# Optimization experiments

Measured on AMD Instinct MI355X. Metric: run time of the kernel, lower is better.

## Reference

```python
import jax, jax.numpy as jnp
import numpy as np

B, S, D, H = 2, 2048, 1024, 16
HD = D // H                      # head_dim = 64
F_POLY = HD + HD * HD            # 4160 degree-2 poly feature dim
M_HID = 2 * D                    # memory_expansion = 2
FFN_H = int(D * 4 * 2 / 3)       # 2730 SwiGLU hidden
GG_H = 64                        # gamma-gate hidden dim
EPS = 1e-6
OMEGA_W, OMEGA_DECAY = 64, 0.95
TTL_ALPHA, TTL_ETA, NS_ITERS = 0.999, 0.01, 5


def rmsnorm(x, w):
    return x * jax.lax.rsqrt(jnp.mean(x * x, -1, keepdims=True) + EPS) * w


def apply_rope(q, k):
    half = HD // 2
    inv = 1.0 / (10000.0 ** (jnp.arange(half, dtype=jnp.float32) / half))
    fr = jnp.arange(S, dtype=jnp.float32)[:, None] * inv[None, :]  # (S, half)
    cos, sin = jnp.cos(fr), jnp.sin(fr)
    def rot(x):
        x1, x2 = x[..., :half], x[..., half:]
        return jnp.concatenate([x1 * cos - x2 * sin, x1 * sin + x2 * cos], -1)
    return rot(q), rot(k)


def phi2(z):
    # degree-2 polynomial features: [z, vec(z z^T)/sqrt(d)]  -> capacity O(d_k^2)
    outer = (z[..., :, None] * z[..., None, :]).reshape(*z.shape[:-1], HD * HD)
    return jnp.concatenate([z, outer / jnp.sqrt(jnp.float32(HD))], -1)


def memory_forward(x, wk, w1, w2):
    feat = phi2(x @ wk)                     # (B,S,F_POLY)
    return jax.nn.silu(feat @ w1) @ w2      # (B,S,D)


def newton_schulz(G):
    # Muon-style quintic Newton-Schulz orthogonalization
    a, b, c = 3.4445, -4.7750, 2.0315
    X = G / (jnp.linalg.norm(G) + 1e-7)
    tall = X.shape[0] > X.shape[1]
    X = X.T if tall else X
    for _ in range(NS_ITERS):
        A = X @ X.T
        X = a * X + (b * A + c * (A @ A)) @ X
    return X.T if tall else X


def block_forward(x, norm1_w, norm2_w, qkv_w, q_norm_w, k_norm_w,
                  gamma_w1, gamma_w2, mem_wk, mem_w1, mem_w2,
                  memory_gate, wo_w, ffn_w1, ffn_w2, ffn_w3):
    h = rmsnorm(x, norm1_w)
    q, k, v = jnp.split(h @ qkv_w, 3, axis=-1)
    heads = lambda t: t.reshape(B, S, H, HD).transpose(0, 2, 1, 3)  # (B,H,S,HD)
    q, k, v = heads(q), heads(k), heads(v)
    q = rmsnorm(q, q_norm_w)   # qk-norm per head
    k = rmsnorm(k, k_norm_w)
    q, k = apply_rope(q, k)

    # input-dependent gamma gate (B,S,1)
    gamma = jax.nn.sigmoid(jax.nn.silu(h @ gamma_w1) @ gamma_w2)

    # causal QK memory projection: gamma-blended causal mean of keys
    k_cummean = jnp.cumsum(k, axis=2) / jnp.arange(1, S + 1, dtype=k.dtype)[None, None, :, None]
    g = gamma[:, None, :, :]                          # (B,1,S,1)
    q_mem = g * q + (1.0 - g) * k_cummean             # (B,H,S,HD)
    q_mem_flat = q_mem.transpose(0, 2, 1, 3).reshape(B, S, D)
    v_flat = v.transpose(0, 2, 1, 3).reshape(B, S, D)

    # --- TTL: Omega-rule loss + Newton-Schulz update of memory params ---
    pos = jnp.arange(S)
    dpow = jnp.float32(OMEGA_DECAY) ** (S - 1 - pos).astype(jnp.float32)
    dpow = jnp.where(pos >= S - OMEGA_W, dpow, 0.0)   # context-window pruning
    w_omega = gamma[..., 0] * dpow                    # (B,S)

    def omega_loss(wk, w1, w2):
        pred = memory_forward(q_mem_flat, wk, w1, w2)
        per_tok = jnp.sum((pred - v_flat) ** 2, -1)   # (B,S)
        return jnp.sum(w_omega * per_tok) / (jnp.sum(w_omega) + 1e-8)

    gk, g1, g2 = jax.grad(omega_loss, argnums=(0, 1, 2))(mem_wk, mem_w1, mem_w2)
    # momentum S_t = theta*0 + grad (fresh state), update M = alpha*M - eta*NS(S_t)
    mem_wk_u = TTL_ALPHA * mem_wk - TTL_ETA * newton_schulz(gk)
    mem_w1_u = TTL_ALPHA * mem_w1 - TTL_ETA * newton_schulz(g1)
    mem_w2_u = TTL_ALPHA * mem_w2 - TTL_ETA * newton_schulz(g2)

    # --- SWA branch (full causal attention) ---
    attn = jnp.einsum('bhsd,bhtd->bhst', q, k) * (HD ** -0.5)
    causal = jnp.tril(jnp.ones((S, S), dtype=bool))
    attn = jnp.where(causal, attn, -jnp.inf)
    attn = jax.nn.softmax(attn, -1)
    attn_out = jnp.einsum('bhst,bhtd->bhsd', attn, v)
    attn_out = attn_out.transpose(0, 2, 1, 3).reshape(B, S, D) @ wo_w

    # --- memory branch with learned output-level gate ---
    mem_out = memory_forward(q_mem_flat, mem_wk_u, mem_w1_u, mem_w2_u)
    mem_out = jax.nn.sigmoid(memory_gate) * mem_out

    x = x + attn_out + mem_out
    h2 = rmsnorm(x, norm2_w)
    x = x + (jax.nn.silu(h2 @ ffn_w1) * (h2 @ ffn_w3)) @ ffn_w2
    return x


def setup_inputs() -> dict:
    key = jax.random.key(0)
    ks = jax.random.split(key, 16)
    std = 0.02
    return {
        'x': jax.random.normal(ks[0], (B, S, D), jnp.float32),
        'norm1_w': jnp.ones((D,), jnp.float32),
        'norm2_w': jnp.ones((D,), jnp.float32),
        'qkv_w': jax.random.normal(ks[1], (D, 3 * D), jnp.float32) * std,
        'q_norm_w': jnp.ones((HD,), jnp.float32),
        'k_norm_w': jnp.ones((HD,), jnp.float32),
        'gamma_w1': jax.random.normal(ks[2], (D, GG_H), jnp.float32) * std,
        'gamma_w2': jnp.zeros((GG_H, 1), jnp.float32),  # zero-init -> gamma ~ 0.5
        'mem_wk': jax.random.normal(ks[3], (D, HD), jnp.float32) * std,
        'mem_w1': jax.random.normal(ks[4], (F_POLY, M_HID), jnp.float32) * std,
        'mem_w2': jax.random.normal(ks[5], (M_HID, D), jnp.float32) * std,
        'memory_gate': jnp.zeros((1,), jnp.float32),    # layer 0 -> pre-sigmoid 0.0
        'wo_w': jax.random.normal(ks[6], (D, D), jnp.float32) * (std / 2 ** 0.5),
        'ffn_w1': jax.random.normal(ks[7], (D, FFN_H), jnp.float32) * std,
        'ffn_w2': jax.random.normal(ks[8], (FFN_H, D), jnp.float32) * std,
        'ffn_w3': jax.random.normal(ks[9], (D, FFN_H), jnp.float32) * std,
    }


def reference(x, norm1_w, norm2_w, qkv_w, q_norm_w, k_norm_w, gamma_w1, gamma_w2,
              mem_wk, mem_w1, mem_w2, memory_gate, wo_w, ffn_w1, ffn_w2, ffn_w3):
    return block_forward(x, norm1_w, norm2_w, qkv_w, q_norm_w, k_norm_w,
                         gamma_w1, gamma_w2, mem_wk, mem_w1, mem_w2,
                         memory_gate, wo_w, ffn_w1, ffn_w2, ffn_w3)
```

## Files before the change

kernel.cpp:

```cpp
#include <hip/hip_runtime.h>
#include <math.h>

#define Bc 2
#define Sc 2048
#define Dc 1024
#define Hc 16
#define HDc 64
#define FPOLY 4160
#define MHID 2048
#define FFNH 2730
#define FFNHP 2752
#define GGH 64
#define NTOK 4096
#define NACT 128

typedef __bf16 bf16;
typedef __attribute__((ext_vector_type(8))) __bf16 bf16x8;
typedef __attribute__((ext_vector_type(4))) float f32x4;

#define AS1 __attribute__((address_space(1)))
#define AS3 __attribute__((address_space(3)))

__device__ __forceinline__ void gload16(const void* g, void* l) {
    __builtin_amdgcn_global_load_lds((AS1 const void*)g, (AS3 void*)l, 16, 0, 0);
// ... 66 lines not shown
    };
    stage(0, 0);
    __syncthreads();
    int buf = 0;
    for (int k0 = 32; k0 < K; k0 += 32) {
        stage(buf ^ 1, k0);
        compute(buf);
        __syncthreads();
        buf ^= 1;
    }
    compute(buf);
    const float amul = alpha * (sptr ? *sptr : 1.f);
#pragma unroll
    for (int nt = 0; nt < 4; ++nt) {
        const int col = bn + wn + nt * 16 + lrow;
        if (col >= N) continue;
#pragma unroll
        for (int mt = 0; mt < 4; ++mt) {
            const int rbase = bm + wm + mt * 16 + q * 4;
#pragma unroll
            for (int r = 0; r < 4; ++r) {
                const size_t o = (size_t)(rbase + r) * ldc + col;
                float v = amul * acc[mt][nt][r];
                if (beta != 0.f)
                    v += beta * (CINBF ? (float)((const bf16*)Cin)[o] : ((const float*)Cin)[o]);
                if (act == 1) v = v / (1.f + __expf(-v));
                if (OUTBF) ((bf16*)Cout)[o] = (bf16)v;
                else       ((float*)Cout)[o] = v;
            }
        }
    }
}

template<int OUTBF, int CINBF>
__global__ __launch_bounds__(256) void gemm_direct(
    const bf16* __restrict__ A, const bf16* __restrict__ Bt,
    const void* __restrict__ Cin, void* __restrict__ Cout,
    int M, int N, int K, int ldc,
    float alpha, float beta, int act, const float* __restrict__ sptr)
{
    const int tid = threadIdx.x, w = tid >> 6, lane = tid & 63;
    const int lrow = lane & 15, quad = lane >> 4;
    const int bm = blockIdx.y * 128 + w * 32;
    const int bn = blockIdx.x * 128;
    f32x4 acc[2][8];
#pragma unroll
    for (int mt = 0; mt < 2; ++mt)
#pragma unroll
        for (int nt = 0; nt < 8; ++nt) { acc[mt][nt][0] = 0.f; acc[mt][nt][1] = 0.f; acc[mt][nt][2] = 0.f; acc[mt][nt][3] = 0.f; }
    const bf16* Abase = A + (size_t)(bm + lrow) * K + quad * 8;
    const bf16* Bbase = Bt + (size_t)(bn + lrow) * K + quad * 8;
#pragma unroll 2
    for (int k0 = 0; k0 < K; k0 += 32) {
        bf16x8 af0 = *(const bf16x8*)(Abase + k0);
        bf16x8 af1 = *(const bf16x8*)(Abase + (size_t)16 * K + k0);
#pragma unroll
        for (int nt = 0; nt < 8; ++nt) {
            bf16x8 bfr = *(const bf16x8*)(Bbase + (size_t)nt * 16 * K + k0);
            acc[0][nt] = __builtin_amdgcn_mfma_f32_16x16x32_bf16(af0, bfr, acc[0][nt], 0, 0, 0);
            acc[1][nt] = __builtin_amdgcn_mfma_f32_16x16x32_bf16(af1, bfr, acc[1][nt], 0, 0, 0);
        }
    }
    const float amul = alpha * (sptr ? *sptr : 1.f);
#pragma unroll
    for (int nt = 0; nt < 8; ++nt) {
        const int col = bn + nt * 16 + lrow;
        if (col >= N) continue;
#pragma unroll
        for (int mt = 0; mt < 2; ++mt) {
            const int rbase = bm + mt * 16 + quad * 4;
#pragma unroll
            for (int r = 0; r < 4; ++r) {
                const int row = rbase + r;
                if (row >= M) continue;
                const size_t o = (size_t)row * ldc + col;
                float v = amul * acc[mt][nt][r];
                if (beta != 0.f)
                    v += beta * (CINBF ? (float)((const bf16*)Cin)[o] : ((const float*)Cin)[o]);
                if (act == 1) v = v / (1.f + __expf(-v));
                if (OUTBF) ((bf16*)Cout)[o] = (bf16)v;
                else       ((float*)Cout)[o] = v;
            }
        }
    }
}

__global__ __launch_bounds__(256) void gemm_skp(
    const bf16* __restrict__ A, const bf16* __restrict__ Bt,
    float* __restrict__ part, int M, int N, int K, int KC)
{
    const int tid = threadIdx.x, w = tid >> 6, lane = tid & 63;
    const int lrow = lane & 15, quad = lane >> 4;
    const int bm = blockIdx.y * 128 + w * 32;
    const int bn = blockIdx.x * 128;
    const int z = blockIdx.z;
    const int kb = z * KC;
    int ke = kb + KC; if (ke > K) ke = K;
    f32x4 acc[2][8];
#pragma unroll
    for (int mt = 0; mt < 2; ++mt)
#pragma unroll
        for (int nt = 0; nt < 8; ++nt) { acc[mt][nt][0] = 0.f; acc[mt][nt][1] = 0.f; acc[mt][nt][2] = 0.f; acc[mt][nt][3] = 0.f; }
    const bf16* Abase = A + (size_t)(bm + lrow) * K + quad * 8;
    const bf16* Bbase = Bt + (size_t)(bn + lrow) * K + quad * 8;
#pragma unroll 2
    for (int k0 = kb; k0 < ke; k0 += 32) {
        bf16x8 af0 = *(const bf16x8*)(Abase + k0);
        bf16x8 af1 = *(const bf16x8*)(Abase + (size_t)16 * K + k0);
#pragma unroll
        for (int nt = 0; nt < 8; ++nt) {
            bf16x8 bfr = *(const bf16x8*)(Bbase + (size_t)nt * 16 * K + k0);
            acc[0][nt] = __builtin_amdgcn_mfma_f32_16x16x32_bf16(af0, bfr, acc[0][nt], 0, 0, 0);
            acc[1][nt] = __builtin_amdgcn_mfma_f32_16x16x32_bf16(af1, bfr, acc[1][nt], 0, 0, 0);
        }
    }
    float* po = part + (size_t)z * M * N;
#pragma unroll
    for (int nt = 0; nt < 8; ++nt) {
        const int col = bn + nt * 16 + lrow;
        if (col >= N) continue;
#pragma unroll
        for (int mt = 0; mt < 2; ++mt) {
            const int rbase = bm + mt * 16 + quad * 4;
#pragma unroll
            for (int r = 0; r < 4; ++r) {
                const int row = rbase + r;
                if (row >= M) continue;
                po[(size_t)row * N + col] = acc[mt][nt][r];
            }
        }
    }
}

__global__ void skred(const float* __restrict__ part, float* __restrict__ out,
                      int SK, int MN)
{
    int i = blockIdx.x * 256 + threadIdx.x;
    if (i >= MN) return;
    float s = 0.f;
    for (int z = 0; z < SK; ++z) s += part[(size_t)z * MN + i];
    out[i] = s;
}

__global__ __launch_bounds__(256) void gram_bat(
    const bf16* __restrict__ X0, const bf16* __restrict__ X1,
    const bf16* __restrict__ X2, const bf16* __restrict__ X3,
    const bf16* __restrict__ X4, float* __restrict__ part)
{
    const int z = blockIdx.x, m = blockIdx.y;
    const bf16* A; int K;
    if      (m == 0) { A = X0; K = 2048; }
    else if (m == 1) { A = X1; K = 1024; }
    else if (m == 2) { A = X2; K = 2048; }
    else if (m == 3) { A = X3; K = 1024; }
    else             { A = X4; K = 64;   }
    if (z * 64 >= K) return;
    const int tid = threadIdx.x, w = tid >> 6, lane = tid & 63;
    const int lrow = lane & 15, quad = lane >> 4;
    const int bm = w * 32;
    f32x4 acc[2][8];
#pragma unroll
    for (int mt = 0; mt < 2; ++mt)
#pragma unroll
        for (int nt = 0; nt < 8; ++nt) { acc[mt][nt][0] = 0.f; acc[mt][nt][1] = 0.f; acc[mt][nt][2] = 0.f; acc[mt][nt][3] = 0.f; }
    const bf16* Abase = A + (size_t)(bm + lrow) * K + quad * 8;
    const bf16* Bbase = A + (size_t)lrow * K + quad * 8;
#pragma unroll 2
    for (int k0 = z * 64; k0 < z * 64 + 64; k0 += 32) {
        bf16x8 af0 = *(const bf16x8*)(Abase + k0);
        bf16x8 af1 = *(const bf16x8*)(Abase + (size_t)16 * K + k0);
#pragma unroll
        for (int nt = 0; nt < 8; ++nt) {
            bf16x8 bfr = *(const bf16x8*)(Bbase + (size_t)nt * 16 * K + k0);
            acc[0][nt] = __builtin_amdgcn_mfma_f32_16x16x32_bf16(af0, bfr, acc[0][nt], 0, 0, 0);
// ... 177 lines not shown
                for (int nt = 0; nt < 8; ++nt)
#pragma unroll
                    for (int r = 0; r < 4; ++r) {
                        const int row = bm + mt * 16 + quad * 4 + r, col = nt * 16 + lrow;
                        Fc[(size_t)row * 128 + col] = (bf16)acc[mt][nt][r];
                    }
        }
        gemm_ll(Cl, FTl);
#pragma unroll
        for (int mt = 0; mt < 2; ++mt)
#pragma unroll
            for (int nt = 0; nt < 8; ++nt)
#pragma unroll
                for (int r = 0; r < 4; ++r) {
                    const int row = bm + mt * 16 + quad * 4 + r, col = nt * 16 + lrow;
                    Ml[swz(col, row)] = (bf16)acc[mt][nt][r];
                }
        __syncthreads();
        gemm_ll(Ml, FTl);
#pragma unroll
        for (int mt = 0; mt < 2; ++mt)
#pragma unroll
            for (int nt = 0; nt < 8; ++nt)
#pragma unroll
                for (int r = 0; r < 4; ++r) {
                    const int row = bm + mt * 16 + quad * 4 + r, col = nt * 16 + lrow;
                    Cl[swz(row, col)] = (bf16)acc[mt][nt][r];
                }
        __syncthreads();
    }
}

__global__ __launch_bounds__(256) void tconv_kernel(
    const float* __restrict__ W, bf16* __restrict__ Wt, int K, int N, int Kpad)
{
    __shared__ float t[32][33];
    const int k0 = blockIdx.x * 32, n0 = blockIdx.y * 32;
    const int tx = threadIdx.x & 31, ty = threadIdx.x >> 5;
#pragma unroll
    for (int r = 0; r < 4; ++r) {
        int gk = k0 + ty + r * 8, gn = n0 + tx;
        t[ty + r * 8][tx] = (gk < K && gn < N) ? W[(size_t)gk * N + gn] : 0.f;
    }
    __syncthreads();
#pragma unroll
    for (int r = 0; r < 4; ++r) {
        int gn = n0 + ty + r * 8, gk = k0 + tx;
        if (gn < N && gk < Kpad) Wt[(size_t)gn * Kpad + gk] = (bf16)t[tx][ty + r * 8];
    }
}

__global__ __launch_bounds__(256) void tconv6_kernel(
    const float* __restrict__ s0, const float* __restrict__ s1,
    const float* __restrict__ s2, const float* __restrict__ s3,
    const float* __restrict__ s4, const float* __restrict__ s5,
    bf16* __restrict__ d0, bf16* __restrict__ d1, bf16* __restrict__ d2,
    bf16* __restrict__ d3, bf16* __restrict__ d4, bf16* __restrict__ d5)
{
    const int zz = blockIdx.z;
    const float* W; bf16* Wt; int N;
    if      (zz == 0) { W = s0; Wt = d0; N = 2048; }
    else if (zz == 1) { W = s1; Wt = d1; N = 1024; }
    else if (zz == 2) { W = s2; Wt = d2; N = 64;   }
    else if (zz == 3) { W = s3; Wt = d3; N = 1024; }
    else if (zz == 4) { W = s4; Wt = d4; N = 4160; }
    else              { W = s5; Wt = d5; N = 2048; }
    const int k0 = blockIdx.x * 32, n0 = blockIdx.y * 32;
    if (n0 >= N) return;
    __shared__ float t[32][33];
    const int tx = threadIdx.x & 31, ty = threadIdx.x >> 5;
#pragma unroll
    for (int r = 0; r < 4; ++r) {
        int gk = k0 + ty + r * 8, gn = n0 + tx;
        t[ty + r * 8][tx] = (gk < 128 && gn < N) ? W[(size_t)gk * N + gn] : 0.f;
    }
    __syncthreads();
#pragma unroll
    for (int r = 0; r < 4; ++r) {
        int gn = n0 + ty + r * 8, gk = k0 + tx;
        if (gn < N) Wt[(size_t)gn * 128 + gk] = (bf16)t[tx][ty + r * 8];
    }
}

__global__ void cvt_kernel(const float* __restrict__ in, bf16* __restrict__ out, int n)
{
    for (int i = blockIdx.x * 256 + threadIdx.x; i < n; i += gridDim.x * 256)
        out[i] = (bf16)in[i];
}

__global__ __launch_bounds__(256) void vtrans_kernel(
    const bf16* __restrict__ qkv, bf16* __restrict__ vt)
{
    __shared__ bf16 t[32][33];
    const int s0 = blockIdx.x * 32, d0 = blockIdx.y * 32, bh = blockIdx.z;
    const int b = bh >> 4, h = bh & 15;
    const int tx = threadIdx.x & 31, ty = threadIdx.x >> 5;
#pragma unroll
    for (int r = 0; r < 4; ++r) {
        int s = s0 + ty + r * 8;
        t[ty + r * 8][tx] = qkv[((size_t)b * Sc + s) * 3072 + 2048 + h * 64 + d0 + tx];
    }
    __syncthreads();
#pragma unroll
    for (int r = 0; r < 4; ++r) {
        int d = d0 + ty + r * 8;
        vt[((size_t)bh * 64 + d) * Sc + s0 + tx] = t[tx][ty + r * 8];
    }
}

__global__ __launch_bounds__(256) void rms_rows(
    const float* __restrict__ in, const float* __restrict__ w,
    bf16* __restrict__ out, int D)
{
    const int row = blockIdx.x;
    const float* r = in + (size_t)row * D;
    bf16* o = out + (size_t)row * D;
    float s = 0.f;
    for (int i = threadIdx.x; i < D; i += 256) { float v = r[i]; s += v * v; }
    __shared__ float red[256];
    red[threadIdx.x] = s;
    __syncthreads();
    for (int st = 128; st; st >>= 1) {
// ... 28 lines not shown
    const int h = y & 15, which = y >> 4;
    const float* w = which ? kw : qw;
    bf16* dst = which ? kd : qd;
    const size_t row = ((size_t)b * Sc + s) * 3072 + which * 1024 + h * 64;
    float v = (float)src[row + lane];
    float ss = v * v;
#pragma unroll
    for (int off = 32; off; off >>= 1) ss += __shfl_xor(ss, off);
    v = v * rsqrtf(ss / 64.f + 1e-6f) * w[lane];
    const int j = lane & 31;
    float inv = powf(10000.f, -(float)j / 32.f);
    float ang = (float)s * inv;
    float sn = sinf(ang), cs = cosf(ang);
    float p = __shfl_xor(v, 32);
    float o;
    if (lane < 32) o = v * cs - p * sn;
    else           o = p * sn + v * cs;
    const size_t od = (((size_t)b * Hc + h) * Sc + s) * 64 + lane;
    dst[od] = (bf16)o;
}

__global__ void kpsum_kernel(const bf16* __restrict__ kn, float* __restrict__ psum)
{
    const int bh = blockIdx.x, c = blockIdx.y, d = threadIdx.x;
    const size_t base = (size_t)bh * Sc * 64 + (size_t)c * 128 * 64 + d;
    float s = 0.f;
    for (int i = 0; i < 128; ++i) s += (float)kn[base + (size_t)i * 64];
    psum[((size_t)bh * 16 + c) * 64 + d] = s;
}

__global__ void qmem2_kernel(
    const bf16* __restrict__ qn, const bf16* __restrict__ kn,
    const float* __restrict__ gamma, const float* __restrict__ psum,
    float* __restrict__ qmem)
{
    const int bh = blockIdx.x, c = blockIdx.y;
    const int b = bh >> 4, hh = bh & 15;
    const int d = threadIdx.x;
    const size_t base = (size_t)bh * Sc * 64;
    float run = 0.f;
    for (int cc = 0; cc < c; ++cc) run += psum[((size_t)bh * 16 + cc) * 64 + d];
    for (int s = c * 128; s < c * 128 + 128; ++s) {
        run += (float)kn[base + (size_t)s * 64 + d];
        float cm = run / (float)(s + 1);
        float g = gamma[b * Sc + s];
        float qv = (float)qn[base + (size_t)s * 64 + d];
        qmem[((size_t)(b * Sc + s)) * Dc + hh * 64 + d] = g * qv + (1.f - g) * cm;
    }
}

__global__ __launch_bounds__(256, 4) void attn_mfma(
    const bf16* __restrict__ qn, const bf16* __restrict__ kn,
    const bf16* __restrict__ vt, bf16* __restrict__ outp)
{
    const int flat = blockIdx.x;
    const int glow = flat & 7, t2 = flat >> 3;
    const int xq = t2 & 31, ghigh = t2 >> 5;
    const int g = glow | (ghigh << 3);
    const int h = g & 15, b = g >> 4;
    const int bh = b * Hc + h;
    const int tid = threadIdx.x, w = tid >> 6, lane = tid & 63;
    const int lrow = lane & 15, quad = lane >> 4;
    const int rhalf = w & 1, pgrp = w >> 1;
    __shared__ bf16 Ps[4][16][136];
    __shared__ float Ob[2][16][68];
    __shared__ float Lb[2][16];
    const bf16* kbase = kn + (size_t)bh * Sc * 64;
    const bf16* vtb = vt + (size_t)bh * 64 * Sc;
    const float SC = 0.1803368801f;
#pragma unroll 1
    for (int ti = 0; ti < 2; ++ti) {
        const int zt = ti ? (63 - xq) : xq;
        const int qb = zt * 32;
        const int nc = (qb >> 7) + 1;
        const int par = pgrp ^ ti;
        const int rowg = qb + rhalf * 16 + quad * 4;
        bf16x8 qf[2];
        const bf16* qbase = qn + ((size_t)bh * Sc + qb + rhalf * 16) * 64;
#pragma unroll
        for (int ks = 0; ks < 2; ++ks)
// ... 110 lines not shown
    __shared__ float red[128];
    red[t] = v; __syncthreads();
    for (int st = 64; st; st >>= 1) { if (t < st) red[t] += red[t + st]; __syncthreads(); }
    if (t == 0) wsum[0] = red[0];
}

__global__ __launch_bounds__(256) void phi2_f32(
    const float* __restrict__ z, float* __restrict__ feat, bf16* __restrict__ featb)
{
    const int f = blockIdx.x * 256 + threadIdx.x;
    const int t = blockIdx.y;
    if (f >= FPOLY) return;
    const float* zr = z + (size_t)t * 64;
    float v;
    if (f < 64) v = zr[f];
    else { int i = (f - 64) >> 6, j = (f - 64) & 63; v = zr[i] * zr[j] * 0.125f; }
    feat[(size_t)t * FPOLY + f] = v;
    featb[(size_t)t * FPOLY + f] = (bf16)v;
}

__global__ __launch_bounds__(256) void phi2_bf16(
    const float* __restrict__ z, bf16* __restrict__ feat)
{
    const int f = blockIdx.x * 256 + threadIdx.x;
    const int t = blockIdx.y;
    if (f >= FPOLY) return;
    const float* zr = z + (size_t)t * 64;
    float v;
    if (f < 64) v = zr[f];
    else { int i = (f - 64) >> 6, j = (f - 64) & 63; v = zr[i] * zr[j] * 0.125f; }
    feat[(size_t)t * FPOLY + f] = (bf16)v;
}

__global__ void silu_kernel(const float* __restrict__ in, float* __restrict__ out,
                            bf16* __restrict__ outb, int n)
{
    int i = blockIdx.x * 256 + threadIdx.x;
    if (i < n) {
        float v = in[i];
        float s = v / (1.f + expf(-v));
        out[i] = s; outb[i] = (bf16)s;
    }
}

__global__ void dpred_kernel(const float* __restrict__ pred, const float* __restrict__ va,
                             const float* __restrict__ wvec, const float* __restrict__ wsum,
                             float* __restrict__ dpred, bf16* __restrict__ dpredb)
{
    int i = blockIdx.x * 256 + threadIdx.x;
    if (i < NACT * Dc) {
        int t = i >> 10;
        float v = 2.f * wvec[t] / (wsum[0] + 1e-8f) * (pred[i] - va[i]);
        dpred[i] = v; dpredb[i] = (bf16)v;
    }
}

__global__ void dsilu_kernel(const float* __restrict__ dsu, const float* __restrict__ u,
                             float* __restrict__ du, bf16* __restrict__ dub, int n)
{
    int i = blockIdx.x * 256 + threadIdx.x;
    if (i < n) {
        float uv = u[i];
        float sg = 1.f / (1.f + expf(-uv));
        float v = dsu[i] * sg * (1.f + uv * (1.f - sg));
        du[i] = v; dub[i] = (bf16)v;
    }
}

__global__ void dz_kernel(const float* __restrict__ dfeat, const float* __restrict__ za,
                          float* __restrict__ dz, bf16* __restrict__ dzb)
{
    const int t = blockIdx.x;
    const int k = threadIdx.x;
    const float* df = dfeat + (size_t)t * FPOLY;
    const float* z = za + (size_t)t * 64;
    float s1 = 0.f, s2 = 0.f;
    for (int j = 0; j < 64; ++j) {
        float zj = z[j];
        s1 += df[64 + k * 64 + j] * zj;
        s2 += df[64 + j * 64 + k] * zj;
    }
    float v = df[k] + 0.125f * (s1 + s2);
    dz[(size_t)t * 64 + k] = v;
    dzb[(size_t)t * 64 + k] = (bf16)v;
}

__global__ void sgate_kernel(const float* __restrict__ mg, float* __restrict__ out)
{
    out[0] = 1.f / (1.f + expf(-mg[0]));
}

__global__ void swiglu_pack(const bf16* __restrict__ u, bf16* __restrict__ o)
{
    int i = blockIdx.x * 256 + threadIdx.x;
    if (i >= NTOK * FFNHP) return;
    int t = i / FFNHP, k = i % FFNHP;
    if (k >= FFNH) { o[i] = (bf16)0.f; return; }
    float a = (float)u[(size_t)t * 5504 + k];
    float b = (float)u[(size_t)t * 5504 + 2752 + k];
    o[i] = (bf16)(a / (1.f + __expf(-a)) * b);
}
// ... 39 lines not shown
    float* x2 = (float*)slabBC;
    bf16* qmemb = (bf16*)slabD;
    bf16* t1b4  = (bf16*)slabD;
    bf16* attnb = (bf16*)slabF;
    bf16* hb = (bf16*)slabG;      bf16* mw1b = (bf16*)slabG;
    bf16* w1uT = (bf16*)slabG;    bf16* h2b = (bf16*)slabG;
    bf16* qkvb = (bf16*)takeB(25165824);
    bf16* ffpk = qkvb;

    bf16* qkvwT = (bf16*)takeB(6291456);
    bf16* gw1T  = (bf16*)takeB(262144);
    bf16* wowT  = (bf16*)takeB(2097152);
    bf16* mw1T  = (bf16*)takeB(17039360);
    bf16* mw2T  = (bf16*)takeB(4194304);
    bf16* fw13T = (bf16*)takeB(11272192);
    bf16* fw2T  = (bf16*)takeB(5636096);
    bf16* mw2b  = (bf16*)takeB(4194304);
    bf16* mwkTb = (bf16*)takeB(262144);
    bf16* wkuTb = (bf16*)takeB(262144);
    bf16* w2uT  = (bf16*)takeB(4194304);

    float* zf    = (float*)takeB(1048576);
    float* gg1   = (float*)takeB(1048576);
    float* gamma = (float*)takeB(16384);
    float* wvec  = (float*)takeB(512);
    float* scal  = (float*)takeB(256);
    float* psum  = (float*)takeB(131072);
    float* xa    = (float*)takeB(524288);
    float* va    = (float*)takeB(524288);
    float* za    = (float*)takeB(32768);
    float* featA = (float*)takeB(2129920);
    float* ua    = (float*)takeB(1048576);
    float* sua   = (float*)takeB(1048576);
    float* preda = (float*)takeB(524288);
    float* dpreda= (float*)takeB(524288);
    float* dsua  = (float*)takeB(1048576);
    float* dua   = (float*)takeB(1048576);
    float* dfeata= (float*)takeB(2129920);
    float* dza   = (float*)takeB(32768);
    float* SA    = (float*)takeB(196608);
    float* CA    = (float*)takeB(196608);
    bf16* featAb = (bf16*)takeB(1064960);
    bf16* suab   = (bf16*)takeB(524288);
    bf16* xab    = (bf16*)takeB(262144);
    bf16* duab   = (bf16*)takeB(524288);
    bf16* dpredab= (bf16*)takeB(262144);
    bf16* dzab   = (bf16*)takeB(16384);
    bf16* PT1Tb  = (bf16*)takeB(524288);
    bf16* PT2Tb  = (bf16*)takeB(262144);
    bf16* PT3Tb  = (bf16*)takeB(32768);
    bf16* duaTb  = (bf16*)takeB(524288);
    bf16* dpredaTb=(bf16*)takeB(262144);
    bf16* dzaTb  = (bf16*)takeB(32768);
    bf16* xaTb   = (bf16*)takeB(262144);
    bf16* featATb= (bf16*)takeB(1081344);
    bf16* suaTb  = (bf16*)takeB(524288);
    bf16* Sb16  = (bf16*)takeB(98304);
    bf16* Cb16  = (bf16*)takeB(98304);
    bf16* FcAb  = (bf16*)takeB(98304);
    bf16* FcTAb = (bf16*)takeB(98304);

    auto gemmB = [&](int outbf, int cinbf, const bf16* A, const bf16* Bt,
                     const void* Cin, void* C, int M, int N, int K, int ldc,
                     float alpha, float beta, int act, const float* sptr) {
        dim3 grid((N + 127) / 128, M / 128);
        if (outbf && cinbf) gemm_bt<1, 1><<<grid, 256, 0, stream>>>(A, Bt, Cin, C, M, N, K, ldc, alpha, beta, act, sptr);
        else if (outbf)     gemm_bt<1, 0><<<grid, 256, 0, stream>>>(A, Bt, Cin, C, M, N, K, ldc, alpha, beta, act, sptr);
        else                gemm_bt<0, 0><<<grid, 256, 0, stream>>>(A, Bt, Cin, C, M, N, K, ldc, alpha, beta, act, sptr);
    };
    auto gdir = [&](int outbf, int cinbf, const bf16* A, const bf16* Bt,
                    const void* Cin, void* C, int M, int N, int K, int ldc,
                    float alpha, float beta, int act, const float* sptr) {
        dim3 grid((N + 127) / 128, (M + 127) / 128);
        if (outbf && cinbf)      gemm_direct<1, 1><<<grid, 256, 0, stream>>>(A, Bt, Cin, C, M, N, K, ldc, alpha, beta, act, sptr);
        else if (outbf)          gemm_direct<1, 0><<<grid, 256, 0, stream>>>(A, Bt, Cin, C, M, N, K, ldc, alpha, beta, act, sptr);
        else if (cinbf)          gemm_direct<0, 1><<<grid, 256, 0, stream>>>(A, Bt, Cin, C, M, N, K, ldc, alpha, beta, act, sptr);
        else                     gemm_direct<0, 0><<<grid, 256, 0, stream>>>(A, Bt, Cin, C, M, N, K, ldc, alpha, beta, act, sptr);
    };
    auto skp = [&](const bf16* A, const bf16* Bt, float* out,
                   int M, int N, int K, int KC) {
        int SK = (K + KC - 1) / KC;
        gemm_skp<<<dim3((N + 127) / 128, (M + 127) / 128, SK), 256, 0, stream>>>(A, Bt, partA, M, N, K, KC);
        int MN = M * N;
        skred<<<(MN + 255) / 256, 256, 0, stream>>>(partA, out, SK, MN);
    };
    auto tconv = [&](const float* W, bf16* Wt, int K, int N, int Kpad) {
        tconv_kernel<<<dim3((Kpad + 31) / 32, (N + 31) / 32), 256, 0, stream>>>(W, Wt, K, N, Kpad);
    };

    tconv(qkvw, qkvwT, Dc, 3 * Dc, Dc);
    tconv(gw1, gw1T, Dc, GGH, Dc);
    tconv(wow, wowT, Dc, Dc, Dc);
    tconv(mw1, mw1T, FPOLY, MHID, FPOLY);
    tconv(mw2, mw2T, MHID, Dc, MHID);
    tconv(fw1, fw13T, Dc, FFNH, Dc);
    tconv(fw3, fw13T + (size_t)2752 * Dc, Dc, FFNH, Dc);
    tconv(fw2, fw2T, FFNH, Dc, FFNHP);
    tconv(mwk, mwkTb, Dc, HDc, Dc);
    cvt_kernel<<<2048, 256, 0, stream>>>(mw2, mw2b, MHID * Dc);
    sgate_kernel<<<1, 1, 0, stream>>>(mgate, scal + 2);

    rms_rows<<<NTOK, 256, 0, stream>>>(x, n1w, hb, Dc);
    gemmB(1, 0, hb, qkvwT, nullptr, qkvb, NTOK, 3 * Dc, Dc, 3 * Dc, 1.f, 0.f, 0, nullptr);
    snr_qk<<<dim3(Sc / 4, 32, Bc), 256, 0, stream>>>(qkvb, qnw, knw, qnb, knb);
    skp(hb, gw1T, gg1, NTOK, GGH, Dc, 256);
    gamma_kernel<<<NTOK / 4, 256, 0, stream>>>(gg1, gw2, gamma);
    cvt_kernel<<<2048, 256, 0, stream>>>(mw1, mw1b, FPOLY * MHID);

    vtrans_kernel<<<dim3(Sc / 32, 2, Bc * Hc), 256, 0, stream>>>(qkvb, vt);
    kpsum_kernel<<<dim3(Bc * Hc, 16), 64, 0, stream>>>(knb, psum);
    qmem2_kernel<<<dim3(Bc * Hc, 16), 64, 0, stream>>>(qnb, knb, gamma, psum, qmem);
    attn_mfma<<<dim3(1024), 256, 0, stream>>>(qnb, knb, vt, attnb);

    gather_active<<<NACT, 256, 0, stream>>>(qmem, qkvb, xa, xab, va);
    wvec_kernel<<<1, 128, 0, stream>>>(gamma, wvec, scal);

    skp(xab, mwkTb, za, NACT, HDc, Dc, 64);
    phi2_f32<<<dim3((FPOLY + 255) / 256, NACT), 256, 0, stream>>>(za, featA, featAb);
    skp(featAb, mw1T, ua, NACT, MHID, FPOLY, 288);
    silu_kernel<<<(NACT * MHID + 255) / 256, 256, 0, stream>>>(ua, sua, suab, NACT * MHID);
    skp(suab, mw2T, preda, NACT, Dc, MHID, 128);
    dpred_kernel<<<(NACT * Dc + 255) / 256, 256, 0, stream>>>(preda, va, wvec, scal, dpreda, dpredab);
    skp(dpredab, mw2b, dsua, NACT, MHID, Dc, 128);
    dsilu_kernel<<<(NACT * MHID + 255) / 256, 256, 0, stream>>>(dsua, ua, dua, duab, NACT * MHID);
    skp(duab, mw1b, dfeata, NACT, FPOLY, MHID, 256);
    dz_kernel<<<NACT, 64, 0, stream>>>(dfeata, za, dza, dzab);

    tconv6_kernel<<<dim3(4, 130, 6), 256, 0, stream>>>(
        dua, dpreda, dza, xa, featA, sua,
        duaTb, dpredaTb, dzaTb, xaTb, featATb, suaTb);

    gram_trick<<<1, 256, 0, stream>>>(za, SA);
    gram_bat<<<dim3(32, 5), 256, 0, stream>>>(suab, xab, duab, dpredab, dzab, partA);
    gram_red<<<320, 256, 0, stream>>>(partA, SA, CA);
    ns_norm_kernel<<<3, 256, 0, stream>>>(SA, CA, Sb16, Cb16, scal + 8);
    ns_fused<<<3, 256, 0, stream>>>(Sb16, Cb16, FcAb, FcTAb);
    gdir(1, 0, duaTb,    FcTAb,         nullptr, PT1Tb, MHID, 128, 128, 128, 1.f, 0.f, 0, scal + 8);
    gdir(1, 0, dpredaTb, FcTAb + 16384, nullptr, PT2Tb, Dc,   128, 128, 128, 1.f, 0.f, 0, scal + 9);
    gdir(1, 0, dzaTb,    FcTAb + 32768, nullptr, PT3Tb, HDc,  128, 128, 128, 1.f, 0.f, 0, scal + 10);

    gdir(1, 1, PT3Tb, xaTb, mwkTb, wkuTb, HDc, Dc, 128, Dc, -0.01f, 0.999f, 0, nullptr);
    gemmB(1, 1, PT1Tb, featATb, mw1T, w1uT, MHID, FPOLY, 128, FPOLY, -0.01f, 0.999f, 0, nullptr);
    gemmB(1, 1, PT2Tb, suaTb, mw2T, w2uT, Dc, MHID, 128, MHID, -0.01f, 0.999f, 0, nullptr);

    gemmB(0, 0, attnb, wowT, x, x2, NTOK, Dc, Dc, Dc, 1.f, 1.f, 0, nullptr);
    cvt_kernel<<<2048, 256, 0, stream>>>(qmem, qmemb, NTOK * Dc);
    gdir(0, 0, qmemb, wkuTb, nullptr, zf, NTOK, HDc, Dc, HDc, 1.f, 0.f, 0, nullptr);

    phi2_bf16<<<dim3((FPOLY + 255) / 256, NTOK), 256, 0, stream>>>(zf, featC4);
    gemmB(1, 0, featC4, w1uT, nullptr, t1b4, NTOK, MHID, FPOLY, MHID, 1.f, 0.f, 1, nullptr);
    gemmB(0, 0, t1b4, w2uT, x2, x2, NTOK, Dc, MHID, Dc, 1.f, 1.f, 0, scal + 2);

    rms_rows<<<NTOK, 256, 0, stream>>>(x2, n2w, h2b, Dc);
    gemmB(1, 0, h2b, fw13T, nullptr, ff13b, NTOK, 5482, Dc, 5504, 1.f, 0.f, 0, nullptr);
    swiglu_pack<<<(NTOK * FFNHP + 255) / 256, 256, 0, stream>>>(ff13b, ffpk);
    gemmB(0, 0, ffpk, fw2T, x2, outp, NTOK, Dc, FFNHP, Dc, 1.f, 1.f, 0, nullptr);
}
```

Baseline: 1.281 ms.

## Fuse elementwise ops into split-K reductions, add 128x64 GEMM, merge small launches

Adds a 128x64-tile GEMM with XCD-aware block swizzling and double-buffered LDS loads. It replaces the 128x128 GEMMs that have N=1024 output (wo, mem w2, ffn w2), giving more workgroups to fill the CUs. The silu, dpred and dsilu elementwise kernels are fused into the split-K reduction kernels. The fp32-to-bf16 weight conversions are folded into the transpose kernels, qmem's bf16 copy is written directly, and three small GEMMs are merged into one launch. The aim is fewer launches and less memory traffic, at the cost of more specialised kernels with hard-coded split counts.

```diff
diff --git a/kernel.cpp b/kernel.cpp
--- a/kernel.cpp
+++ b/kernel.cpp
@@ -122,6 +122,97 @@
     }
 }
 
+__global__ __launch_bounds__(256) void gemm_bt64(
+    const bf16* __restrict__ A, const bf16* __restrict__ Bt,
+    const float* __restrict__ Cin, float* __restrict__ Cout,
+    int M, int N, int K, int ldc, const float* __restrict__ sptr)
+{
+    __shared__ bf16 As[2][128 * 32];
+    __shared__ bf16 Bs[2][64 * 32];
+    const int tid = threadIdx.x;
+    const int w = tid >> 6, lane = tid & 63;
+    const int gridX = gridDim.x;
+    const int nwg = gridX * gridDim.y;
+    const int orig = blockIdx.y * gridX + blockIdx.x;
+    const int q8 = nwg >> 3, r8 = nwg & 7;
+    const int xcd = orig & 7, lid = orig >> 3;
+    const int sbase = (xcd < r8) ? xcd * (q8 + 1) : r8 * (q8 + 1) + (xcd - r8) * q8;
+    const int swzid = sbase + lid;
+    const int bm = (swzid / gridX) * 128, bn = (swzid % gridX) * 64;
+    const int wm = w * 32;
+    f32x4 acc[2][4];
+#pragma unroll
+    for (int i = 0; i < 2; ++i)
+#pragma unroll
+        for (int j = 0; j < 4; ++j) { acc[i][j][0] = 0.f; acc[i][j][1] = 0.f; acc[i][j][2] = 0.f; acc[i][j][3] = 0.f; }
+    const int idx0 = tid, idx1 = tid + 256;
+    const int r0 = idx0 >> 2, r1 = idx1 >> 2;
+    const int g0 = ((idx0 & 3) ^ ((r0 >> 1) & 3)) * 8;
+    const int g1 = ((idx1 & 3) ^ ((r1 >> 1) & 3)) * 8;
+    const int rB = tid >> 2;
+    const int gB = ((tid & 3) ^ ((rB >> 1) & 3)) * 8;
+    const int lrow = lane & 15;
+    const int q = lane >> 4;
+    int aoff[2], boff[4];
+#pragma unroll
+    for (int t = 0; t < 2; ++t) {
+        int ar = wm + t * 16 + lrow;
+        aoff[t] = ar * 32 + ((q ^ ((ar >> 1) & 3)) * 8);
+    }
+#pragma unroll
+    for (int nt = 0; nt < 4; ++nt) {
+        int br = nt * 16 + lrow;
+        boff[nt] = br * 32 + ((q ^ ((br >> 1) & 3)) * 8);
+    }
+    const bf16* Arow0 = A + (size_t)(bm + r0) * K + g0;
+    const bf16* Arow1 = A + (size_t)(bm + r1) * K + g1;
+    const bf16* Brow  = Bt + (size_t)(bn + rB) * K + gB;
+    auto stage = [&](int bi, int k0) {
+        char* la = (char*)&As[bi][0] + w * 1024;
+        char* lb = (char*)&Bs[bi][0] + w * 1024;
+        gload16(Arow0 + k0, la);
+        gload16(Arow1 + k0, la + 4096);
+        gload16(Brow + k0, lb);
+    };
+    auto compute = [&](int bi) {
+        bf16x8 af[2], bfr[4];
+#pragma unroll
+        for (int t = 0; t < 2; ++t) af[t] = *(const bf16x8*)&As[bi][aoff[t]];
+#pragma unroll
+        for (int nt = 0; nt < 4; ++nt) bfr[nt] = *(const bf16x8*)&Bs[bi][boff[nt]];
+#pragma unroll
+        for (int mt = 0; mt < 2; ++mt)
+#pragma unroll
+            for (int nt = 0; nt < 4; ++nt)
+                acc[mt][nt] = __builtin_amdgcn_mfma_f32_16x16x32_bf16(af[mt], bfr[nt], acc[mt][nt], 0, 0, 0);
+    };
+    stage(0, 0);
+    __syncthreads();
+    int buf = 0;
+    for (int k0 = 32; k0 < K; k0 += 32) {
+        stage(buf ^ 1, k0);
+        compute(buf);
+        __syncthreads();
+        buf ^= 1;
+    }
+    compute(buf);
+    const float amul = sptr ? *sptr : 1.f;
+#pragma unroll
+    for (int nt = 0; nt < 4; ++nt) {
+        const int col = bn + nt * 16 + lrow;
+        if (col >= N) continue;
+#pragma unroll
+        for (int mt = 0; mt < 2; ++mt) {
+            const int rbase = bm + wm + mt * 16 + q * 4;
+#pragma unroll
+            for (int r = 0; r < 4; ++r) {
+                const size_t o = (size_t)(rbase + r) * ldc + col;
+                Cout[o] = amul * acc[mt][nt][r] + Cin[o];
+            }
+        }
+    }
+}
+
 template<int OUTBF, int CINBF>
 __global__ __launch_bounds__(256) void gemm_direct(
     const bf16* __restrict__ A, const bf16* __restrict__ Bt,
@@ -175,6 +266,55 @@
     }
 }
 
+__global__ __launch_bounds__(256) void gdir3_kernel(
+    const bf16* __restrict__ A0, const bf16* __restrict__ A1, const bf16* __restrict__ A2,
+    const bf16* __restrict__ B0, bf16* __restrict__ C0, bf16* __restrict__ C1,
+    bf16* __restrict__ C2, const float* __restrict__ invn)
+{
+    const int z = blockIdx.z;
+    const bf16* A; const bf16* Bt; bf16* C; int M;
+    if      (z == 0) { A = A0; Bt = B0;         C = C0; M = 2048; }
+    else if (z == 1) { A = A1; Bt = B0 + 16384; C = C1; M = 1024; }
+    else             { A = A2; Bt = B0 + 32768; C = C2; M = 64;   }
+    if (blockIdx.y * 128 >= M) return;
+    const float s = invn[z];
+    const int tid = threadIdx.x, w = tid >> 6, lane = tid & 63;
+    const int lrow = lane & 15, quad = lane >> 4;
+    const int bm = blockIdx.y * 128 + w * 32;
+    f32x4 acc[2][8];
+#pragma unroll
+    for (int mt = 0; mt < 2; ++mt)
+#pragma unroll
+        for (int nt = 0; nt < 8; ++nt) { acc[mt][nt][0] = 0.f; acc[mt][nt][1] = 0.f; acc[mt][nt][2] = 0.f; acc[mt][nt][3] = 0.f; }
+    const bf16* Abase = A + (size_t)(bm + lrow) * 128 + quad * 8;
+    const bf16* Bbase = Bt + (size_t)lrow * 128 + quad * 8;
+#pragma unroll
+    for (int k0 = 0; k0 < 128; k0 += 32) {
+        bf16x8 af0 = *(const bf16x8*)(Abase + k0);
+        bf16x8 af1 = *(const bf16x8*)(Abase + (size_t)16 * 128 + k0);
+#pragma unroll
+        for (int nt = 0; nt < 8; ++nt) {
+            bf16x8 bfr = *(const bf16x8*)(Bbase + (size_t)nt * 16 * 128 + k0);
+            acc[0][nt] = __builtin_amdgcn_mfma_f32_16x16x32_bf16(af0, bfr, acc[0][nt], 0, 0, 0);
+            acc[1][nt] = __builtin_amdgcn_mfma_f32_16x16x32_bf16(af1, bfr, acc[1][nt], 0, 0, 0);
+        }
+    }
+#pragma unroll
+    for (int nt = 0; nt < 8; ++nt) {
+        const int col = nt * 16 + lrow;
+#pragma unroll
+        for (int mt = 0; mt < 2; ++mt) {
+            const int rbase = bm + mt * 16 + quad * 4;
+#pragma unroll
+            for (int r = 0; r < 4; ++r) {
+                const int row = rbase + r;
+                if (row >= M) continue;
+                C[(size_t)row * 128 + col] = (bf16)(s * acc[mt][nt][r]);
+            }
+        }
+    }
+}
+
 __global__ __launch_bounds__(256) void gemm_skp(
     const bf16* __restrict__ A, const bf16* __restrict__ Bt,
     float* __restrict__ part, int M, int N, int K, int KC)
@@ -230,6 +370,44 @@
     float s = 0.f;
     for (int z = 0; z < SK; ++z) s += part[(size_t)z * MN + i];
     out[i] = s;
+}
+
+__global__ void skred_silu(const float* __restrict__ part, float* __restrict__ ua,
+                           float* __restrict__ sua, bf16* __restrict__ suab)
+{
+    int i = blockIdx.x * 256 + threadIdx.x;
+    if (i >= NACT * MHID) return;
+    float s = 0.f;
+    for (int z = 0; z < 15; ++z) s += part[(size_t)z * NACT * MHID + i];
+    ua[i] = s;
+    float sg = s / (1.f + expf(-s));
+    sua[i] = sg; suab[i] = (bf16)sg;
+}
+
+__global__ void skred_dpred(const float* __restrict__ part, const float* __restrict__ va,
+                            const float* __restrict__ wvec, const float* __restrict__ wsum,
+                            float* __restrict__ dpred, bf16* __restrict__ dpredb)
+{
+    int i = blockIdx.x * 256 + threadIdx.x;
+    if (i >= NACT * Dc) return;
+    float s = 0.f;
+    for (int z = 0; z < 16; ++z) s += part[(size_t)z * NACT * Dc + i];
+    int t = i >> 10;
+    float v = 2.f * wvec[t] / (wsum[0] + 1e-8f) * (s - va[i]);
+    dpred[i] = v; dpredb[i] = (bf16)v;
+}
+
+__global__ void skred_dsilu(const float* __restrict__ part, const float* __restrict__ u,
+                            float* __restrict__ du, bf16* __restrict__ dub)
+{
+    int i = blockIdx.x * 256 + threadIdx.x;
+    if (i >= NACT * MHID) return;
+    float s = 0.f;
+    for (int z = 0; z < 8; ++z) s += part[(size_t)z * NACT * MHID + i];
+    float uv = u[i];
+    float sg = 1.f / (1.f + expf(-uv));
+    float v = s * sg * (1.f + uv * (1.f - sg));
+    du[i] = v; dub[i] = (bf16)v;
 }
 
 __global__ __launch_bounds__(256) void gram_bat(
@@ -473,7 +651,8 @@
 }
 
 __global__ __launch_bounds__(256) void tconv_kernel(
-    const float* __restrict__ W, bf16* __restrict__ Wt, int K, int N, int Kpad)
+    const float* __restrict__ W, bf16* __restrict__ Wt, int K, int N, int Kpad,
+    bf16* __restrict__ Wc)
 {
     __shared__ float t[32][33];
     const int k0 = blockIdx.x * 32, n0 = blockIdx.y * 32;
@@ -481,7 +660,10 @@
 #pragma unroll
     for (int r = 0; r < 4; ++r) {
         int gk = k0 + ty + r * 8, gn = n0 + tx;
-        t[ty + r * 8][tx] = (gk < K && gn < N) ? W[(size_t)gk * N + gn] : 0.f;
+        bool ok = (gk < K && gn < N);
+        float v = ok ? W[(size_t)gk * N + gn] : 0.f;
+        t[ty + r * 8][tx] = v;
+        if (Wc && ok) Wc[(size_t)gk * N + gn] = (bf16)v;
     }
     __syncthreads();
 #pragma unroll
@@ -523,12 +705,6 @@
     }
 }
 
-__global__ void cvt_kernel(const float* __restrict__ in, bf16* __restrict__ out, int n)
-{
-    for (int i = blockIdx.x * 256 + threadIdx.x; i < n; i += gridDim.x * 256)
-        out[i] = (bf16)in[i];
-}
-
 __global__ __launch_bounds__(256) void vtrans_kernel(
     const bf16* __restrict__ qkv, bf16* __restrict__ vt)
 {
@@ -623,7 +799,7 @@
 __global__ void qmem2_kernel(
     const bf16* __restrict__ qn, const bf16* __restrict__ kn,
     const float* __restrict__ gamma, const float* __restrict__ psum,
-    float* __restrict__ qmem)
+    float* __restrict__ qmem, bf16* __restrict__ qmemb)
 {
     const int bh = blockIdx.x, c = blockIdx.y;
     const int b = bh >> 4, hh = bh & 15;
@@ -636,7 +812,10 @@
         float cm = run / (float)(s + 1);
         float g = gamma[b * Sc + s];
         float qv = (float)qn[base + (size_t)s * 64 + d];
-        qmem[((size_t)(b * Sc + s)) * Dc + hh * 64 + d] = g * qv + (1.f - g) * cm;
+        float val = g * qv + (1.f - g) * cm;
+        const size_t o = ((size_t)(b * Sc + s)) * Dc + hh * 64 + d;
+        qmem[o] = val;
+        qmemb[o] = (bf16)val;
     }
 }
 
@@ -813,41 +992,6 @@
     feat[(size_t)t * FPOLY + f] = (bf16)v;
 }
 
-__global__ void silu_kernel(const float* __restrict__ in, float* __restrict__ out,
-                            bf16* __restrict__ outb, int n)
-{
-    int i = blockIdx.x * 256 + threadIdx.x;
-    if (i < n) {
-        float v = in[i];
-        float s = v / (1.f + expf(-v));
-        out[i] = s; outb[i] = (bf16)s;
-    }
-}
-
-__global__ void dpred_kernel(const float* __restrict__ pred, const float* __restrict__ va,
-                             const float* __restrict__ wvec, const float* __restrict__ wsum,
-                             float* __restrict__ dpred, bf16* __restrict__ dpredb)
-{
-    int i = blockIdx.x * 256 + threadIdx.x;
-    if (i < NACT * Dc) {
-        int t = i >> 10;
-        float v = 2.f * wvec[t] / (wsum[0] + 1e-8f) * (pred[i] - va[i]);
-        dpred[i] = v; dpredb[i] = (bf16)v;
-    }
-}
-
-__global__ void dsilu_kernel(const float* __restrict__ dsu, const float* __restrict__ u,
-                             float* __restrict__ du, bf16* __restrict__ dub, int n)
-{
-    int i = blockIdx.x * 256 + threadIdx.x;
-    if (i < n) {
-        float uv = u[i];
-        float sg = 1.f / (1.f + expf(-uv));
-        float v = dsu[i] * sg * (1.f + uv * (1.f - sg));
-        du[i] = v; dub[i] = (bf16)v;
-    }
-}
-
 __global__ void dz_kernel(const float* __restrict__ dfeat, const float* __restrict__ za,
                           float* __restrict__ dz, bf16* __restrict__ dzb)
 {
@@ -953,9 +1097,7 @@
     float* featA = (float*)takeB(2129920);
     float* ua    = (float*)takeB(1048576);
     float* sua   = (float*)takeB(1048576);
-    float* preda = (float*)takeB(524288);
     float* dpreda= (float*)takeB(524288);
-    float* dsua  = (float*)takeB(1048576);
     float* dua   = (float*)takeB(1048576);
     float* dfeata= (float*)takeB(2129920);
     float* dza   = (float*)takeB(32768);
@@ -989,6 +1131,11 @@
         else if (outbf)     gemm_bt<1, 0><<<grid, 256, 0, stream>>>(A, Bt, Cin, C, M, N, K, ldc, alpha, beta, act, sptr);
         else                gemm_bt<0, 0><<<grid, 256, 0, stream>>>(A, Bt, Cin, C, M, N, K, ldc, alpha, beta, act, sptr);
     };
+    auto gemm64 = [&](const bf16* A, const bf16* Bt, const float* Cin, float* C,
+                      int M, int N, int K, int ldc, const float* sptr) {
+        dim3 grid(N / 64, M / 128);
+        gemm_bt64<<<grid, 256, 0, stream>>>(A, Bt, Cin, C, M, N, K, ldc, sptr);
+    };
     auto gdir = [&](int outbf, int cinbf, const bf16* A, const bf16* Bt,
                     const void* Cin, void* C, int M, int N, int K, int ldc,
                     float alpha, float beta, int act, const float* sptr) {
@@ -1005,20 +1152,18 @@
         int MN = M * N;
         skred<<<(MN + 255) / 256, 256, 0, stream>>>(partA, out, SK, MN);
     };
-    auto tconv = [&](const float* W, bf16* Wt, int K, int N, int Kpad) {
-        tconv_kernel<<<dim3((Kpad + 31) / 32, (N + 31) / 32), 256, 0, stream>>>(W, Wt, K, N, Kpad);
+    auto tconv = [&](const float* W, bf16* Wt, int K, int N, int Kpad, bf16* Wc) {
+        tconv_kernel<<<dim3((Kpad + 31) / 32, (N + 31) / 32), 256, 0, stream>>>(W, Wt, K, N, Kpad, Wc);
     };
 
-    tconv(qkvw, qkvwT, Dc, 3 * Dc, Dc);
-    tconv(gw1, gw1T, Dc, GGH, Dc);
-    tconv(wow, wowT, Dc, Dc, Dc);
-    tconv(mw1, mw1T, FPOLY, MHID, FPOLY);
-    tconv(mw2, mw2T, MHID, Dc, MHID);
-    tconv(fw1, fw13T, Dc, FFNH, Dc);
-    tconv(fw3, fw13T + (size_t)2752 * Dc, Dc, FFNH, Dc);
-    tconv(fw2, fw2T, FFNH, Dc, FFNHP);
-    tconv(mwk, mwkTb, Dc, HDc, Dc);
-    cvt_kernel<<<2048, 256, 0, stream>>>(mw2, mw2b, MHID * Dc);
+    tconv(qkvw, qkvwT, Dc, 3 * Dc, Dc, nullptr);
+    tconv(gw1, gw1T, Dc, GGH, Dc, nullptr);
+    tconv(wow, wowT, Dc, Dc, Dc, nullptr);
+    tconv(mw2, mw2T, MHID, Dc, MHID, mw2b);
+    tconv(fw1, fw13T, Dc, FFNH, Dc, nullptr);
+    tconv(fw3, fw13T + (size_t)2752 * Dc, Dc, FFNH, Dc, nullptr);
+    tconv(fw2, fw2T, FFNH, Dc, FFNHP, nullptr);
+    tconv(mwk, mwkTb, Dc, HDc, Dc, nullptr);
     sgate_kernel<<<1, 1, 0, stream>>>(mgate, scal + 2);
 
     rms_rows<<<NTOK, 256, 0, stream>>>(x, n1w, hb, Dc);
@@ -1026,11 +1171,11 @@
     snr_qk<<<dim3(Sc / 4, 32, Bc), 256, 0, stream>>>(qkvb, qnw, knw, qnb, knb);
     skp(hb, gw1T, gg1, NTOK, GGH, Dc, 256);
     gamma_kernel<<<NTOK / 4, 256, 0, stream>>>(gg1, gw2, gamma);
-    cvt_kernel<<<2048, 256, 0, stream>>>(mw1, mw1b, FPOLY * MHID);
+    tconv(mw1, mw1T, FPOLY, MHID, FPOLY, mw1b);
 
     vtrans_kernel<<<dim3(Sc / 32, 2, Bc * Hc), 256, 0, stream>>>(qkvb, vt);
     kpsum_kernel<<<dim3(Bc * Hc, 16), 64, 0, stream>>>(knb, psum);
-    qmem2_kernel<<<dim3(Bc * Hc, 16), 64, 0, stream>>>(qnb, knb, gamma, psum, qmem);
+    qmem2_kernel<<<dim3(Bc * Hc, 16), 64, 0, stream>>>(qnb, knb, gamma, psum, qmem, qmemb);
     attn_mfma<<<dim3(1024), 256, 0, stream>>>(qnb, knb, vt, attnb);
 
     gather_active<<<NACT, 256, 0, stream>>>(qmem, qkvb, xa, xab, va);
@@ -1038,12 +1183,12 @@
 
     skp(xab, mwkTb, za, NACT, HDc, Dc, 64);
     phi2_f32<<<dim3((FPOLY + 255) / 256, NACT), 256, 0, stream>>>(za, featA, featAb);
-    skp(featAb, mw1T, ua, NACT, MHID, FPOLY, 288);
-    silu_kernel<<<(NACT * MHID + 255) / 256, 256, 0, stream>>>(ua, sua, suab, NACT * MHID);
-    skp(suab, mw2T, preda, NACT, Dc, MHID, 128);
-    dpred_kernel<<<(NACT * Dc + 255) / 256, 256, 0, stream>>>(preda, va, wvec, scal, dpreda, dpredab);
-    skp(dpredab, mw2b, dsua, NACT, MHID, Dc, 128);
-    dsilu_kernel<<<(NACT * MHID + 255) / 256, 256, 0, stream>>>(dsua, ua, dua, duab, NACT * MHID);
+    gemm_skp<<<dim3(16, 1, 15), 256, 0, stream>>>(featAb, mw1T, partA, NACT, MHID, FPOLY, 288);
+    skred_silu<<<1024, 256, 0, stream>>>(partA, ua, sua, suab);
+    gemm_skp<<<dim3(8, 1, 16), 256, 0, stream>>>(suab, mw2T, partA, NACT, Dc, MHID, 128);
+    skred_dpred<<<512, 256, 0, stream>>>(partA, va, wvec, scal, dpreda, dpredab);
+    gemm_skp<<<dim3(16, 1, 8), 256, 0, stream>>>(dpredab, mw2b, partA, NACT, MHID, Dc, 128);
+    skred_dsilu<<<1024, 256, 0, stream>>>(partA, ua, dua, duab);
     skp(duab, mw1b, dfeata, NACT, FPOLY, MHID, 256);
     dz_kernel<<<NACT, 64, 0, stream>>>(dfeata, za, dza, dzab);
 
@@ -1056,24 +1201,22 @@
     gram_red<<<320, 256, 0, stream>>>(partA, SA, CA);
     ns_norm_kernel<<<3, 256, 0, stream>>>(SA, CA, Sb16, Cb16, scal + 8);
     ns_fused<<<3, 256, 0, stream>>>(Sb16, Cb16, FcAb, FcTAb);
-    gdir(1, 0, duaTb,    FcTAb,         nullptr, PT1Tb, MHID, 128, 128, 128, 1.f, 0.f, 0, scal + 8);
-    gdir(1, 0, dpredaTb, FcTAb + 16384, nullptr, PT2Tb, Dc,   128, 128, 128, 1.f, 0.f, 0, scal + 9);
-    gdir(1, 0, dzaTb,    FcTAb + 32768, nullptr, PT3Tb, HDc,  128, 128, 128, 1.f, 0.f, 0, scal + 10);
+    gdir3_kernel<<<dim3(1, 16, 3), 256, 0, stream>>>(
+        duaTb, dpredaTb, dzaTb, FcTAb, PT1Tb, PT2Tb, PT3Tb, scal + 8);
 
     gdir(1, 1, PT3Tb, xaTb, mwkTb, wkuTb, HDc, Dc, 128, Dc, -0.01f, 0.999f, 0, nullptr);
     gemmB(1, 1, PT1Tb, featATb, mw1T, w1uT, MHID, FPOLY, 128, FPOLY, -0.01f, 0.999f, 0, nullptr);
     gemmB(1, 1, PT2Tb, suaTb, mw2T, w2uT, Dc, MHID, 128, MHID, -0.01f, 0.999f, 0, nullptr);
 
-    gemmB(0, 0, attnb, wowT, x, x2, NTOK, Dc, Dc, Dc, 1.f, 1.f, 0, nullptr);
-    cvt_kernel<<<2048, 256, 0, stream>>>(qmem, qmemb, NTOK * Dc);
-    gdir(0, 0, qmemb, wkuTb, nullptr, zf, NTOK, HDc, Dc, HDc, 1.f, 0.f, 0, nullptr);
+    gemm64(attnb, wowT, x, x2, NTOK, Dc, Dc, Dc, nullptr);
+    skp(qmemb, wkuTb, zf, NTOK, HDc, Dc, 128);
 
     phi2_bf16<<<dim3((FPOLY + 255) / 256, NTOK), 256, 0, stream>>>(zf, featC4);
     gemmB(1, 0, featC4, w1uT, nullptr, t1b4, NTOK, MHID, FPOLY, MHID, 1.f, 0.f, 1, nullptr);
-    gemmB(0, 0, t1b4, w2uT, x2, x2, NTOK, Dc, MHID, Dc, 1.f, 1.f, 0, scal + 2);
+    gemm64(t1b4, w2uT, x2, x2, NTOK, Dc, MHID, Dc, scal + 2);
 
     rms_rows<<<NTOK, 256, 0, stream>>>(x2, n2w, h2b, Dc);
     gemmB(1, 0, h2b, fw13T, nullptr, ff13b, NTOK, 5482, Dc, 5504, 1.f, 0.f, 0, nullptr);
     swiglu_pack<<<(NTOK * FFNHP + 255) / 256, 256, 0, stream>>>(ff13b, ffpk);
-    gemmB(0, 0, ffpk, fw2T, x2, outp, NTOK, Dc, FFNHP, Dc, 1.f, 1.f, 0, nullptr);
-}
+    gemm64(ffpk, fw2T, x2, outp, NTOK, Dc, FFNHP, Dc, nullptr);
+}
```

New measurement: 1.162 ms. 1.1x faster.
